# Performance work log

Measured on AMD Instinct MI355X. Metric: run time of the kernel, lower is better.

## Reference

```python
import jax, jax.numpy as jnp
import numpy as np

B, S, D, H = 8, 1024, 1024, 16
DH = D // H  # head dim = 64 (extend_head=False split)
EPS = 1e-5


def setup_inputs() -> dict:
    key = jax.random.key(0)
    ks = jax.random.split(key, 9)
    s = 0.02
    return {
        "query": jax.random.normal(ks[0], (B, S, D), jnp.float32),
        "key":   jax.random.normal(ks[1], (B, S, D), jnp.float32),
        "value": jax.random.normal(ks[2], (B, S, D), jnp.float32),
        "mask":  jnp.ones((B, S), jnp.bool_),
        # Linear weights stored [in, out] (torch uses [out, in]; math identical)
        "Wq": jax.random.normal(ks[3], (D, D), jnp.float32) * s,
        "bq": jnp.zeros((D,), jnp.float32),
        "Wk": jax.random.normal(ks[4], (D, D), jnp.float32) * s,
        "bk": jnp.zeros((D,), jnp.float32),
        "Wv": jax.random.normal(ks[5], (D, D), jnp.float32) * s,
        "bv": jnp.zeros((D,), jnp.float32),
        # BatchNorm1d affine params
        "gamma": jnp.ones((D,), jnp.float32),
        "beta":  jnp.zeros((D,), jnp.float32),
    }


def _split_heads(x):
    # torch: cat(x.split(DH, -1), 0) -> head-major stacking [H*B, S, DH]
    return x.reshape(B, S, H, DH).transpose(2, 0, 1, 3)  # [H,B,S,DH]


def reference(query, key, value, mask, Wq, bq, Wk, bk, Wv, bv, gamma, beta):
    q = query @ Wq + bq   # [B,S,D]
    k = key   @ Wk + bk
    v = value @ Wv + bv

    qh = _split_heads(q)  # [H,B,S,DH]
    kh = _split_heads(k)
    vh = _split_heads(v)

    # NOTE: source builds an additive mask but never applies it to the
    # scores -> faithful reference uses UNMASKED softmax.
    scores = jnp.einsum('hbqd,hbkd->hbqk', qh, kh) / np.sqrt(DH).astype(np.float32)
    weights = jax.nn.softmax(scores, axis=-1)          # [H,B,S,S]
    out = jnp.einsum('hbqk,hbkd->hbqd', weights, vh)   # [H,B,S,DH]

    # cat(split(out, B, 0), -1): re-concatenate heads on feature dim
    out = out.transpose(1, 2, 0, 3).reshape(B, S, D)

    # row-gather by boolean mask (all-ones -> static shape [B*S, D])
    out = out.reshape(-1, D)[mask.reshape(-1)]

    # BatchNorm1d (training-mode batch stats, biased var) + SiLU
    mean = out.mean(axis=0)
    var = jnp.mean(jnp.square(out - mean), axis=0)
    out = (out - mean) / jnp.sqrt(var + EPS) * gamma + beta
    return jax.nn.silu(out)
```

## Files before the change

### kernel.cpp

```cpp
#include <hip/hip_runtime.h>
#include <hip/hip_bf16.h>
#include <cstdint>
#include <cstddef>

#define B_ 8
#define S_ 1024
#define D_ 1024
#define H_ 16
#define DH_ 64

using f32x4   = __attribute__((ext_vector_type(4))) float;
using f32x16  = __attribute__((ext_vector_type(16))) float;
using float4v = __attribute__((ext_vector_type(4))) float;
using bf16x8  = __attribute__((ext_vector_type(8))) short;
using ushort8 = __attribute__((ext_vector_type(8))) unsigned short;
using uint2v  = __attribute__((ext_vector_type(2))) unsigned int;

__device__ __forceinline__ unsigned short f2bf(float f) {
    union { float f; unsigned u; } v; v.f = f;
    unsigned r = v.u + 0x7FFF + ((v.u >> 16) & 1);
    return (unsigned short)(r >> 16);
}
__device__ __forceinline__ float bf2f(unsigned short b) {
    union { unsigned u; float f; } v; v.u = ((unsigned)b) << 16;
    return v.f;
}

#if __has_builtin(__builtin_amdgcn_exp2f)
__device__ __forceinline__ float fexp2(float x) { return __builtin_amdgcn_exp2f(x); }
#else
__device__ __forceinline__ float fexp2(float x) { return __expf(x * 0.69314718056f); }
#endif

__device__ __forceinline__ unsigned cvtpk_bf16(float lo, float hi) {
    unsigned r;
    asm("v_cvt_pk_bf16_f32 %0, %1, %2" : "=v"(r) : "v"(lo), "v"(hi));
    return r;
}

__device__ __forceinline__ void gl_lds16(const unsigned short* g, unsigned short* l) {
    __builtin_amdgcn_global_load_lds(
        (const __attribute__((address_space(1))) unsigned int*)g,
        (__attribute__((address_space(3))) unsigned int*)l,
        16, 0, 0);
}

__global__ __launch_bounds__(256) void prep_kernel(
    const float* __restrict__ Wq, const float* __restrict__ Wk, const float* __restrict__ Wv,
    const float* __restrict__ Xq, const float* __restrict__ Xk, const float* __restrict__ Xv,
    unsigned short* __restrict__ Wt,
    unsigned short* __restrict__ Bq, unsigned short* __restrict__ Bk, unsigned short* __restrict__ Bv,
    float* __restrict__ gsum)
{
    __shared__ float tile[32][33];
    int bid = blockIdx.x;
    int t = threadIdx.x;

    if (bid == 0) {
#pragma unroll
        for (int j = 0; j < 8; ++j) gsum[t + 256 * j] = 0.f;
    }

    if (bid < 3072) {
        int z = bid >> 10, rc = bid & 1023;
        const float* W = (z == 0) ? Wq : (z == 1) ? Wk : Wv;
        unsigned short* Y = Wt + (size_t)z * 1048576;
        int tx = t & 31, ty = t >> 5;
        int r0 = (rc >> 5) * 32, c0 = (rc & 31) * 32;
#pragma unroll
        for (int j = 0; j < 4; ++j) {
            int r = ty + j * 8;
            tile[r][tx] = W[(size_t)(r0 + r) * D_ + c0 + tx];
        }
        __syncthreads();
#pragma unroll
        for (int j = 0; j < 4; ++j) {
            int r = ty + j * 8;
            Y[(size_t)(c0 + r) * D_ + r0 + tx] = f2bf(tile[tx][r]);
        }
    } else {
        int cid = bid - 3072;
        int which = cid >> 12;
        int blk = cid & 4095;
        const float* X = (which == 0) ? Xq : (which == 1) ? Xk : Xv;
        unsigned short* Y = (which == 0) ? Bq : (which == 1) ? Bk : Bv;
        size_t idx = ((size_t)blk * 256 + t) * 8;
        float4v v0 = *reinterpret_cast<const float4v*>(X + idx);
        float4v v1 = *reinterpret_cast<const float4v*>(X + idx + 4);
        ushort8 o;
#pragma unroll
        for (int j = 0; j < 4; ++j) { o[j] = f2bf(v0[j]); o[j + 4] = f2bf(v1[j]); }
        *reinterpret_cast<ushort8*>(Y + idx) = o;
    }
}

__global__ __launch_bounds__(256, 2) void qkv_gemm8(
    const unsigned short* __restrict__ Xbq, const unsigned short* __restrict__ Xbk, const unsigned short* __restrict__ Xbv,
    const unsigned short* __restrict__ Wts,
    const float* __restrict__ bq, const float* __restrict__ bk, const float* __restrict__ bv,
    unsigned short* __restrict__ Qh, unsigned short* __restrict__ Kf, unsigned short* __restrict__ Vf)
{
    extern __shared__ unsigned short smem[];
    unsigned short* lA = smem;
    unsigned short* lB = smem + 16384;

    int bid = blockIdx.x;
    int L = (bid & 7) * 192 + (bid >> 3);
    int mode = L >> 9;
    int rem = L & 511;
    int bm = rem >> 3;
    int bn = rem & 7;

    const unsigned short* Xb = (mode == 0) ? Xbq : (mode == 1) ? Xbk : Xbv;
    const unsigned short* Wt = Wts + (size_t)mode * 1048576;
    const float* bias = (mode == 0) ? bq : (mode == 1) ? bk : bv;

    int t = threadIdx.x;
    int m0 = bm * 128, n0 = bn * 128;
    int wid = t >> 6, lane = t & 63;
    int wr = wid >> 1, wc = wid & 1;
    int lr = lane & 15, lg = lane >> 4;

    int srow = t >> 3;
    int scol = (((t & 7) ^ (srow & 7))) * 8;
    const unsigned short* Asrc = Xb + (size_t)(m0 + srow) * D_ + scol;
    const unsigned short* Bsrc = Wt + (size_t)(n0 + srow) * D_ + scol;
    unsigned short* lAdst = lA + t * 8;
    unsigned short* lBdst = lB + t * 8;

#define STAGE_A(buf, p, kt) gl_lds16(Asrc + (size_t)(p) * 32 * D_ + (kt) * 64, lAdst + (buf) * 8192 + (p) * 2048)
#define STAGE_B(buf, p, kt) gl_lds16(Bsrc + (size_t)(p) * 32 * D_ + (kt) * 64, lBdst + (buf) * 8192 + (p) * 2048)
#define STAGE_A4(buf, kt) do { STAGE_A(buf,0,kt); STAGE_A(buf,1,kt); STAGE_A(buf,2,kt); STAGE_A(buf,3,kt); } while (0)
#define STAGE_B4(buf, kt) do { STAGE_B(buf,0,kt); STAGE_B(buf,1,kt); STAGE_B(buf,2,kt); STAGE_B(buf,3,kt); } while (0)

#define READ_A(base)                                                                 \
    _Pragma("unroll") for (int m_ = 0; m_ < 4; ++m_) {                               \
        int R_ = wr * 64 + m_ * 16 + lr;                                             \
        _Pragma("unroll") for (int ks_ = 0; ks_ < 2; ++ks_) {                        \
            int pc_ = ((ks_ * 4 + lg) ^ (R_ & 7)) * 8;                               \
            a[m_][ks_] = *reinterpret_cast<const bf16x8*>((base) + R_ * 64 + pc_);   \
        }                                                                            \
    }
#define READ_B2(base, nb)                                                            \
    _Pragma("unroll") for (int n_ = 0; n_ < 2; ++n_) {                               \
        int R_ = wc * 64 + ((nb) + n_) * 16 + lr;                                    \
        _Pragma("unroll") for (int ks_ = 0; ks_ < 2; ++ks_) {                        \
            int pc_ = ((ks_ * 4 + lg) ^ (R_ & 7)) * 8;                               \
            b[n_][ks_] = *reinterpret_cast<const bf16x8*>((base) + R_ * 64 + pc_);   \
        }                                                                            \
    }
#define MFMA_BLK(NB)                                                                 \
    _Pragma("unroll") for (int m_ = 0; m_ < 4; ++m_)                                 \
        _Pragma("unroll") for (int n_ = 0; n_ < 2; ++n_)                             \
            _Pragma("unroll") for (int ks_ = 0; ks_ < 2; ++ks_)                      \
                acc[m_][(NB) + n_] = __builtin_amdgcn_mfma_f32_16x16x32_bf16(        \
                    a[m_][ks_], b[n_][ks_], acc[m_][(NB) + n_], 0, 0, 0);

#define BAR1() do { __builtin_amdgcn_s_barrier();                                    \
                    asm volatile("s_waitcnt lgkmcnt(0)" ::: "memory");               \
                    __builtin_amdgcn_sched_barrier(0);                               \
                    __builtin_amdgcn_s_setprio(1); } while (0)
#define BAR2() do { __builtin_amdgcn_s_setprio(0);                                   \
                    __builtin_amdgcn_s_barrier();                                    \
                    __builtin_amdgcn_sched_barrier(0); } while (0)

    f32x4 acc[4][4] = {};
    bf16x8 a[4][2], b[2][2];

    STAGE_A4(0, 0); STAGE_B4(0, 0);
    STAGE_A4(1, 1);
    asm volatile("s_waitcnt vmcnt(4)" ::: "memory");
    __builtin_amdgcn_s_barrier();
    __builtin_amdgcn_sched_barrier(0);

#pragma unroll 1
    for (int i = 0; i < 8; ++i) {
        int c1 = 2 * i + 1, nt0 = 2 * i + 2, nt1 = 2 * i + 3;
        bool g = (i < 7);
        const unsigned short* A0p = lA;
        const unsigned short* B0p = lB;
        const unsigned short* A1p = lA + 8192;
        const unsigned short* B1p = lB + 8192;

        READ_A(A0p); READ_B2(B0p, 0);
        STAGE_B4(1, c1);
        BAR1(); MFMA_BLK(0); BAR2();

        READ_B2(B0p, 2);
        BAR1(); MFMA_BLK(2);
        __builtin_amdgcn_s_setprio(0);
        if (g) {
            STAGE_A4(0, nt0);
            asm volatile("s_waitcnt vmcnt(4)" ::: "memory");
        } else {
            asm volatile("s_waitcnt vmcnt(0)" ::: "memory");
        }
        __builtin_amdgcn_s_barrier();
        __builtin_amdgcn_sched_barrier(0);

        READ_A(A1p); READ_B2(B1p, 0);
        if (g) STAGE_B4(0, nt0);
        BAR1(); MFMA_BLK(0); BAR2();

        READ_B2(B1p, 2);
        BAR1(); MFMA_BLK(2);
        __builtin_amdgcn_s_setprio(0);
        if (g) {
            STAGE_A4(1, nt1);
            asm volatile("s_waitcnt vmcnt(4)" ::: "memory");
        } else {
            asm volatile("s_waitcnt vmcnt(0)" ::: "memory");
        }
        __builtin_amdgcn_s_barrier();
        __builtin_amdgcn_sched_barrier(0);
    }
#undef BAR1
#undef BAR2
#undef MFMA_BLK
#undef READ_A
#undef READ_B2
#undef STAGE_A
#undef STAGE_B
#undef STAGE_A4
#undef STAGE_B4

#pragma unroll
    for (int am = 0; am < 4; ++am) {
#pragma unroll
        for (int an = 0; an < 4; ++an) {
            int col = n0 + wc * 64 + an * 16 + lr;
            int h = col >> 6, d = col & 63;
            float bval = bias[col];
#pragma unroll
            for (int r = 0; r < 4; ++r) {
                int row = m0 + wr * 64 + am * 16 + lg * 4 + r;
                int bb = row >> 10, s = row & 1023;
                int inst = h * B_ + bb;
                float v = acc[am][an][r] + bval;
                if (mode == 0) {
                    Qh[((size_t)inst * S_ + s) * DH_ + d] = f2bf(v * 0.18033688f);
                } else if (mode == 1) {
                    int kt2 = s >> 6, n_ = (s >> 5) & 1, cl = s & 31;
                    int dk = d >> 4, hi2 = (d >> 3) & 1, j = d & 7;
                    size_t off = ((((size_t)inst * 16 + kt2) * 2 + n_) * 4 + dk) * 512
                               + (size_t)(hi2 * 32 + cl) * 8 + j;
                    Kf[off] = f2bf(v);
                } else {
                    int kt2 = s >> 6, ks2 = (s >> 4) & 3, hi2 = (s >> 3) & 1, j = s & 7;
                    int nd = d >> 5, cl = d & 31;
                    size_t off = ((((size_t)inst * 16 + kt2) * 2 + nd) * 4 + ks2) * 512
                               + (size_t)(hi2 * 32 + cl) * 8 + j;
                    Vf[off] = f2bf(v);
                }
            }
        }
    }
}

__global__ __launch_bounds__(512, 2) void attn_kernel(
    const unsigned short* __restrict__ Qh,
    const unsigned short* __restrict__ Kf,
    const unsigned short* __restrict__ Vf,
    unsigned short* __restrict__ O,
    float* __restrict__ gsum, float* __restrict__ gsq)
{
    __shared__ unsigned short ldsK[2][4096];
    __shared__ unsigned short ldsV[2][4096];
    __shared__ float part[8][64][4];

    int inst = blockIdx.x;
    int h = inst >> 3, bb = inst & 7;
    int t = threadIdx.x, wid = t >> 6, lane = t & 63;
    int cl = lane & 31, hi = lane >> 5;
    int q0 = (blockIdx.y * 8 + wid) * 32;

    const unsigned short* Qb = Qh + (size_t)inst * S_ * DH_ + (size_t)(q0 + cl) * DH_ + hi * 8;
    const unsigned short* Kt = Kf + (size_t)inst * 65536;
    const unsigned short* Vt = Vf + (size_t)inst * 65536;

    bf16x8 qf[4];
#pragma unroll
    for (int dk = 0; dk < 4; ++dk)
        qf[dk] = *reinterpret_cast<const bf16x8*>(Qb + dk * 16);

#define STAGE_KV(buf, kt) do {                                              \
        gl_lds16(Kt + (size_t)(kt) * 4096 + t * 8, &ldsK[buf][t * 8]);      \
        gl_lds16(Vt + (size_t)(kt) * 4096 + t * 8, &ldsV[buf][t * 8]);      \
    } while (0)

    STAGE_KV(0, 0);
    STAGE_KV(1, 1);

    f32x16 o0 = {}, o1 = {};
    float li = 0.f;

#pragma unroll 1
    for (int kt = 0; kt < S_ / 64; ++kt) {
        int buf = kt & 1;
        asm volatile("s_waitcnt vmcnt(2)" ::: "memory");
        __builtin_amdgcn_s_barrier();
        __builtin_amdgcn_sched_barrier(0);

        const unsigned short* kb = &ldsK[buf][0] + lane * 8;
        const unsigned short* vp = &ldsV[buf][0] + lane * 8;

        bf16x8 ka[2][4];
#pragma unroll
        for (int n = 0; n < 2; ++n)
#pragma unroll
            for (int dk = 0; dk < 4; ++dk)
                ka[n][dk] = *reinterpret_cast<const bf16x8*>(kb + (n * 4 + dk) * 512);

        bf16x8 vb0[4], vb1[4];
#pragma unroll
        for (int ks = 0; ks < 4; ++ks) {
            vb0[ks] = *reinterpret_cast<const bf16x8*>(vp + ks * 512);
            vb1[ks] = *reinterpret_cast<const bf16x8*>(vp + (4 + ks) * 512);
        }

        f32x16 s0 = {}, s1 = {};
        __builtin_amdgcn_s_setprio(1);
#pragma unroll
        for (int dk = 0; dk < 4; ++dk)
            s0 = __builtin_amdgcn_mfma_f32_32x32x16_bf16(ka[0][dk], qf[dk], s0, 0, 0, 0);
#pragma unroll
        for (int dk = 0; dk < 4; ++dk)
            s1 = __builtin_amdgcn_mfma_f32_32x32x16_bf16(ka[1][dk], qf[dk], s1, 0, 0, 0);
        __builtin_amdgcn_s_setprio(0);

        float p0[16], p1[16];
#pragma unroll
        for (int i = 0; i < 16; ++i) { p0[i] = fexp2(s0[i]); p1[i] = fexp2(s1[i]); }
        float ts[16];
#pragma unroll
        for (int i = 0; i < 16; ++i) ts[i] = p0[i] + p1[i];
#pragma unroll
        for (int st = 8; st > 0; st >>= 1)
#pragma unroll
            for (int i = 0; i < st; ++i) ts[i] += ts[i + st];
        li += ts[0] + __shfl_xor(ts[0], 32, 64);

        unsigned w[16];
#pragma unroll
        for (int i = 0; i < 8; ++i) w[i]     = cvtpk_bf16(p0[2 * i], p0[2 * i + 1]);
#pragma unroll
        for (int i = 0; i < 8; ++i) w[8 + i] = cvtpk_bf16(p1[2 * i], p1[2 * i + 1]);

        bf16x8 pa[4];
#pragma unroll
        for (int g = 0; g < 4; ++g) {
            uint2v ra = __builtin_amdgcn_permlane32_swap(w[4 * g + 0], w[4 * g + 2], false, false);
            uint2v rb = __builtin_amdgcn_permlane32_swap(w[4 * g + 1], w[4 * g + 3], false, false);
            union { unsigned u[4]; bf16x8 v; } cv;
            cv.u[0] = ra[0]; cv.u[1] = rb[0]; cv.u[2] = ra[1]; cv.u[3] = rb[1];
            pa[g] = cv.v;
        }

        __builtin_amdgcn_s_setprio(1);
#pragma unroll
        for (int g = 0; g < 4; ++g) {
            o0 = __builtin_amdgcn_mfma_f32_32x32x16_bf16(pa[g], vb0[g], o0, 0, 0, 0);
            o1 = __builtin_amdgcn_mfma_f32_32x32x16_bf16(pa[g], vb1[g], o1, 0, 0, 0);
        }
        __builtin_amdgcn_s_setprio(0);

        asm volatile("s_waitcnt lgkmcnt(0)" ::: "memory");
        __builtin_amdgcn_s_barrier();
        __builtin_amdgcn_sched_barrier(0);
        if (kt + 2 < S_ / 64) STAGE_KV(buf, kt + 2);
    }
#undef STAGE_KV

    float rli = 1.0f / li;
    float sa = 0.f, qa = 0.f, sb = 0.f, qb2 = 0.f;
#pragma unroll
    for (int r = 0; r < 16; ++r) {
        int qr = (r & 3) + 8 * (r >> 2) + 4 * hi;
        float inv = __shfl(rli, qr, 64);
        int s = q0 + qr;
        size_t base = ((size_t)bb * S_ + s) * D_ + h * DH_;
        float y0 = o0[r] * inv, y1 = o1[r] * inv;
        O[base + cl]      = f2bf(y0);
        O[base + 32 + cl] = f2bf(y1);
        sa += y0; qa += y0 * y0; sb += y1; qb2 += y1 * y1;
    }
    part[wid][lane][0] = sa; part[wid][lane][1] = qa;
    part[wid][lane][2] = sb; part[wid][lane][3] = qb2;
    __syncthreads();
    if (t < 128) {
        int cl2 = t >> 2, st = t & 3;
        float acc = 0.f;
#pragma unroll
        for (int w2 = 0; w2 < 8; ++w2)
            acc += part[w2][cl2][st] + part[w2][cl2 + 32][st];
        int col = h * 64 + cl2 + ((st >= 2) ? 32 : 0);
        float* tgt = (st & 1) ? gsq : gsum;
        atomicAdd(&tgt[col], acc);
    }
}

__global__ __launch_bounds__(256) void bn_apply(const unsigned short* __restrict__ O,
                                                const float* __restrict__ gsum,
                                                const float* __restrict__ gsq,
                                                const float* __restrict__ gamma,
                                                const float* __restrict__ beta,
                                                float* __restrict__ out) {
    const float invN = 1.f / 8192.f;
    size_t idx = ((size_t)blockIdx.x * 256 + threadIdx.x) * 8;
    int col0 = (int)(idx & 1023);
    ushort8 v = *reinterpret_cast<const ushort8*>(O + idx);
#pragma unroll
    for (int j = 0; j < 8; ++j) {
        int c = col0 + j;
        float mean = gsum[c] * invN;
        float var = gsq[c] * invN - mean * mean;
        float rstd = rsqrtf(var + 1e-5f);
        float x = bf2f(v[j]);
        float y = (x - mean) * rstd * gamma[c] + beta[c];
        out[idx + j] = y / (1.f + __expf(-y));
    }
}

extern "C" void kernel_launch(void* const* d_in, const int* in_sizes, int n_in,
                              void* d_out, int out_size, void* d_ws, size_t ws_size,
                              hipStream_t stream) {
    const float* query = (const float*)d_in[0];
    const float* key   = (const float*)d_in[1];
    const float* value = (const float*)d_in[2];
    const float* Wq = (const float*)d_in[4];
    const float* bq = (const float*)d_in[5];
    const float* Wk = (const float*)d_in[6];
    const float* bk = (const float*)d_in[7];
    const float* Wv = (const float*)d_in[8];
    const float* bv = (const float*)d_in[9];
    const float* gamma = (const float*)d_in[10];
    const float* beta  = (const float*)d_in[11];

    char* w = (char*)d_ws;
    unsigned short* Wt  = (unsigned short*)w;
    unsigned short* Qh  = (unsigned short*)(w + (6u << 20));
    unsigned short* Kf  = Qh + 8388608;
    unsigned short* Vf  = Kf + 8388608;
    unsigned short* Xbq = Vf + 8388608;
    unsigned short* Xbk = Xbq + 8388608;
    unsigned short* Xbv = Xbk + 8388608;
    unsigned short* O   = Xbq;
    float* gsum = (float*)(Xbv + 8388608);
    float* gsq  = gsum + 1024;

    prep_kernel<<<dim3(15360), 256, 0, stream>>>(Wq, Wk, Wv, query, key, value,
                                                 Wt, Xbq, Xbk, Xbv, gsum);

    hipFuncSetAttribute(reinterpret_cast<const void*>(&qkv_gemm8),
                        hipFuncAttributeMaxDynamicSharedMemorySize, 65536);
    qkv_gemm8<<<dim3(1536), 256, 65536, stream>>>(Xbq, Xbk, Xbv, Wt,
                                                  bq, bk, bv, Qh, Kf, Vf);

    attn_kernel<<<dim3(128, 4), 512, 0, stream>>>(Qh, Kf, Vf, O, gsum, gsq);

    bn_apply<<<4096, 256, 0, stream>>>(O, gsum, gsq, gamma, beta, (float*)d_out);
}
```

Baseline: 148.0 us.

## Fuse fp32-to-bf16 activation conversion into QKV GEMM A-tile staging

The separate prep pass that converted query/key/value from fp32 to bf16 in global memory is removed. The GEMM now loads fp32 A tiles into registers, converts them with packed bf16 conversion, and writes them to swizzled LDS, with loads for the next tile issued ahead of time. This drops a full read and write of three activation tensors and one launch's worth of blocks. In exchange the A path no longer uses direct global-to-LDS loads, raises register pressure, and reads twice the bytes per tile, since fp32 is re-read by each of the 8 column blocks.

```diff
diff --git a/kernel.cpp b/kernel.cpp
--- a/kernel.cpp
+++ b/kernel.cpp
@@ -47,10 +47,7 @@
 
 __global__ __launch_bounds__(256) void prep_kernel(
     const float* __restrict__ Wq, const float* __restrict__ Wk, const float* __restrict__ Wv,
-    const float* __restrict__ Xq, const float* __restrict__ Xk, const float* __restrict__ Xv,
-    unsigned short* __restrict__ Wt,
-    unsigned short* __restrict__ Bq, unsigned short* __restrict__ Bk, unsigned short* __restrict__ Bv,
-    float* __restrict__ gsum)
+    unsigned short* __restrict__ Wt, float* __restrict__ gsum)
 {
     __shared__ float tile[32][33];
     int bid = blockIdx.x;
@@ -61,41 +58,26 @@
         for (int j = 0; j < 8; ++j) gsum[t + 256 * j] = 0.f;
     }
 
-    if (bid < 3072) {
-        int z = bid >> 10, rc = bid & 1023;
-        const float* W = (z == 0) ? Wq : (z == 1) ? Wk : Wv;
-        unsigned short* Y = Wt + (size_t)z * 1048576;
-        int tx = t & 31, ty = t >> 5;
-        int r0 = (rc >> 5) * 32, c0 = (rc & 31) * 32;
-#pragma unroll
-        for (int j = 0; j < 4; ++j) {
-            int r = ty + j * 8;
-            tile[r][tx] = W[(size_t)(r0 + r) * D_ + c0 + tx];
-        }
-        __syncthreads();
-#pragma unroll
-        for (int j = 0; j < 4; ++j) {
-            int r = ty + j * 8;
-            Y[(size_t)(c0 + r) * D_ + r0 + tx] = f2bf(tile[tx][r]);
-        }
-    } else {
-        int cid = bid - 3072;
-        int which = cid >> 12;
-        int blk = cid & 4095;
-        const float* X = (which == 0) ? Xq : (which == 1) ? Xk : Xv;
-        unsigned short* Y = (which == 0) ? Bq : (which == 1) ? Bk : Bv;
-        size_t idx = ((size_t)blk * 256 + t) * 8;
-        float4v v0 = *reinterpret_cast<const float4v*>(X + idx);
-        float4v v1 = *reinterpret_cast<const float4v*>(X + idx + 4);
-        ushort8 o;
-#pragma unroll
-        for (int j = 0; j < 4; ++j) { o[j] = f2bf(v0[j]); o[j + 4] = f2bf(v1[j]); }
-        *reinterpret_cast<ushort8*>(Y + idx) = o;
+    int z = bid >> 10, rc = bid & 1023;
+    const float* W = (z == 0) ? Wq : (z == 1) ? Wk : Wv;
+    unsigned short* Y = Wt + (size_t)z * 1048576;
+    int tx = t & 31, ty = t >> 5;
+    int r0 = (rc >> 5) * 32, c0 = (rc & 31) * 32;
+#pragma unroll
+    for (int j = 0; j < 4; ++j) {
+        int r = ty + j * 8;
+        tile[r][tx] = W[(size_t)(r0 + r) * D_ + c0 + tx];
+    }
+    __syncthreads();
+#pragma unroll
+    for (int j = 0; j < 4; ++j) {
+        int r = ty + j * 8;
+        Y[(size_t)(c0 + r) * D_ + r0 + tx] = f2bf(tile[tx][r]);
     }
 }
 
 __global__ __launch_bounds__(256, 2) void qkv_gemm8(
-    const unsigned short* __restrict__ Xbq, const unsigned short* __restrict__ Xbk, const unsigned short* __restrict__ Xbv,
+    const float* __restrict__ Xq, const float* __restrict__ Xk, const float* __restrict__ Xv,
     const unsigned short* __restrict__ Wts,
     const float* __restrict__ bq, const float* __restrict__ bk, const float* __restrict__ bv,
     unsigned short* __restrict__ Qh, unsigned short* __restrict__ Kf, unsigned short* __restrict__ Vf)
@@ -111,7 +93,7 @@
     int bm = rem >> 3;
     int bn = rem & 7;
 
-    const unsigned short* Xb = (mode == 0) ? Xbq : (mode == 1) ? Xbk : Xbv;
+    const float* X = (mode == 0) ? Xq : (mode == 1) ? Xk : Xv;
     const unsigned short* Wt = Wts + (size_t)mode * 1048576;
     const float* bias = (mode == 0) ? bq : (mode == 1) ? bk : bv;
 
@@ -123,15 +105,30 @@
 
     int srow = t >> 3;
     int scol = (((t & 7) ^ (srow & 7))) * 8;
-    const unsigned short* Asrc = Xb + (size_t)(m0 + srow) * D_ + scol;
     const unsigned short* Bsrc = Wt + (size_t)(n0 + srow) * D_ + scol;
-    unsigned short* lAdst = lA + t * 8;
     unsigned short* lBdst = lB + t * 8;
 
-#define STAGE_A(buf, p, kt) gl_lds16(Asrc + (size_t)(p) * 32 * D_ + (kt) * 64, lAdst + (buf) * 8192 + (p) * 2048)
+    int arow = t >> 4;
+    int acolf = (t & 15) * 4;
+    int ag = (t & 15) >> 1;
+    int ahalf = t & 1;
+    const float* Xsrc = X + (size_t)m0 * D_ + acolf;
+
 #define STAGE_B(buf, p, kt) gl_lds16(Bsrc + (size_t)(p) * 32 * D_ + (kt) * 64, lBdst + (buf) * 8192 + (p) * 2048)
-#define STAGE_A4(buf, kt) do { STAGE_A(buf,0,kt); STAGE_A(buf,1,kt); STAGE_A(buf,2,kt); STAGE_A(buf,3,kt); } while (0)
 #define STAGE_B4(buf, kt) do { STAGE_B(buf,0,kt); STAGE_B(buf,1,kt); STAGE_B(buf,2,kt); STAGE_B(buf,3,kt); } while (0)
+
+#define ALOAD(kt)                                                                    \
+    _Pragma("unroll") for (int j_ = 0; j_ < 8; ++j_)                                 \
+        av[j_] = *reinterpret_cast<const float4v*>(Xsrc + (size_t)(arow + 16 * j_) * D_ + (kt) * 64);
+
+#define AWRITE(buf)                                                                  \
+    _Pragma("unroll") for (int j_ = 0; j_ < 8; ++j_) {                               \
+        int r_ = arow + 16 * j_;                                                     \
+        unsigned lo_ = cvtpk_bf16(av[j_][0], av[j_][1]);                             \
+        unsigned hi_ = cvtpk_bf16(av[j_][2], av[j_][3]);                             \
+        uint2v v_; v_[0] = lo_; v_[1] = hi_;                                         \
+        *reinterpret_cast<uint2v*>(lA + (buf) * 8192 + r_ * 64 + ((ag ^ (r_ & 7)) * 8) + ahalf * 4) = v_; \
+    }
 
 #define READ_A(base)                                                                 \
     _Pragma("unroll") for (int m_ = 0; m_ < 4; ++m_) {                               \
@@ -166,12 +163,16 @@
 
     f32x4 acc[4][4] = {};
     bf16x8 a[4][2], b[2][2];
-
-    STAGE_A4(0, 0); STAGE_B4(0, 0);
-    STAGE_A4(1, 1);
-    asm volatile("s_waitcnt vmcnt(4)" ::: "memory");
+    float4v av[8];
+
+    ALOAD(0);
+    AWRITE(0);
+    STAGE_B4(0, 0);
+    asm volatile("s_waitcnt vmcnt(0)" ::: "memory");
+    asm volatile("s_waitcnt lgkmcnt(0)" ::: "memory");
     __builtin_amdgcn_s_barrier();
     __builtin_amdgcn_sched_barrier(0);
+    ALOAD(1);
 
 #pragma unroll 1
     for (int i = 0; i < 8; ++i) {
@@ -187,14 +188,12 @@
         BAR1(); MFMA_BLK(0); BAR2();
 
         READ_B2(B0p, 2);
+        AWRITE(1);
+        if (g) ALOAD(nt0);
         BAR1(); MFMA_BLK(2);
         __builtin_amdgcn_s_setprio(0);
-        if (g) {
-            STAGE_A4(0, nt0);
-            asm volatile("s_waitcnt vmcnt(4)" ::: "memory");
-        } else {
-            asm volatile("s_waitcnt vmcnt(0)" ::: "memory");
-        }
+        if (g) asm volatile("s_waitcnt vmcnt(8)" ::: "memory");
+        else   asm volatile("s_waitcnt vmcnt(0)" ::: "memory");
         __builtin_amdgcn_s_barrier();
         __builtin_amdgcn_sched_barrier(0);
 
@@ -203,14 +202,11 @@
         BAR1(); MFMA_BLK(0); BAR2();
 
         READ_B2(B1p, 2);
+        if (g) { AWRITE(0); ALOAD(nt1); }
         BAR1(); MFMA_BLK(2);
         __builtin_amdgcn_s_setprio(0);
-        if (g) {
-            STAGE_A4(1, nt1);
-            asm volatile("s_waitcnt vmcnt(4)" ::: "memory");
-        } else {
-            asm volatile("s_waitcnt vmcnt(0)" ::: "memory");
-        }
+        if (g) asm volatile("s_waitcnt vmcnt(8)" ::: "memory");
+        else   asm volatile("s_waitcnt vmcnt(0)" ::: "memory");
         __builtin_amdgcn_s_barrier();
         __builtin_amdgcn_sched_barrier(0);
     }
@@ -219,10 +215,10 @@
 #undef MFMA_BLK
 #undef READ_A
 #undef READ_B2
-#undef STAGE_A
 #undef STAGE_B
-#undef STAGE_A4
 #undef STAGE_B4
+#undef ALOAD
+#undef AWRITE
 
 #pragma unroll
     for (int am = 0; am < 4; ++am) {
@@ -441,19 +437,15 @@
     unsigned short* Qh  = (unsigned short*)(w + (6u << 20));
     unsigned short* Kf  = Qh + 8388608;
     unsigned short* Vf  = Kf + 8388608;
-    unsigned short* Xbq = Vf + 8388608;
-    unsigned short* Xbk = Xbq + 8388608;
-    unsigned short* Xbv = Xbk + 8388608;
-    unsigned short* O   = Xbq;
-    float* gsum = (float*)(Xbv + 8388608);
+    unsigned short* O   = Vf + 8388608;
+    float* gsum = (float*)(O + 8388608);
     float* gsq  = gsum + 1024;
 
-    prep_kernel<<<dim3(15360), 256, 0, stream>>>(Wq, Wk, Wv, query, key, value,
-                                                 Wt, Xbq, Xbk, Xbv, gsum);
+    prep_kernel<<<dim3(3072), 256, 0, stream>>>(Wq, Wk, Wv, Wt, gsum);
 
     hipFuncSetAttribute(reinterpret_cast<const void*>(&qkv_gemm8),
                         hipFuncAttributeMaxDynamicSharedMemorySize, 65536);
-    qkv_gemm8<<<dim3(1536), 256, 65536, stream>>>(Xbq, Xbk, Xbv, Wt,
+    qkv_gemm8<<<dim3(1536), 256, 65536, stream>>>(query, key, value, Wt,
                                                   bq, bk, bv, Qh, Kf, Vf);
 
     attn_kernel<<<dim3(128, 4), 512, 0, stream>>>(Qh, Kf, Vf, O, gsum, gsq);
```

After: 146.1 us (median of 4 runs). Within noise of the previous version (-1.3%).
